# Optimization experiments

Measured on AMD Instinct MI355X. Metric: run time of the kernel, lower is better.

The kernel has to match this reference:

```python
import jax, jax.numpy as jnp
import numpy as np
import math

DIM = 1024
H = 16
HD = DIM // H  # 64
M = 64         # num_features
B, S = 4, 4096


def setup_inputs() -> dict:
    key = jax.random.key(0)
    ks = jax.random.split(key, 10)
    sc = 1.0 / math.sqrt(DIM)
    return {
        "x": jax.random.normal(ks[0], (B, S, DIM), dtype=jnp.float32),
        "Wq": jax.random.normal(ks[1], (DIM, DIM), dtype=jnp.float32) * sc,
        "bq": jax.random.normal(ks[2], (DIM,), dtype=jnp.float32) * 0.01,
        "Wk": jax.random.normal(ks[3], (DIM, DIM), dtype=jnp.float32) * sc,
        "bk": jax.random.normal(ks[4], (DIM,), dtype=jnp.float32) * 0.01,
        "Wv": jax.random.normal(ks[5], (DIM, DIM), dtype=jnp.float32) * sc,
        "bv": jax.random.normal(ks[6], (DIM,), dtype=jnp.float32) * 0.01,
        "Wo": jax.random.normal(ks[7], (DIM, DIM), dtype=jnp.float32) * sc,
        "bo": jax.random.normal(ks[8], (DIM,), dtype=jnp.float32) * 0.01,
        "P": jax.random.normal(ks[9], (H, M, HD), dtype=jnp.float32),
    }


def _feature_map(t, P):
    # t: [b,h,s,d], P: [h,m,d] -> relu(t @ P^T) / sqrt(m)
    proj = jnp.einsum("bhsd,hmd->bhsm", t, P)
    return jax.nn.relu(proj) * (1.0 / math.sqrt(P.shape[1]))


def reference(x, Wq, bq, Wk, bk, Wv, bv, Wo, bo, P):
    b, s, dim = x.shape
    h, m, hd = P.shape
    # Linear projections (torch Linear: x @ W^T + b), split heads -> [b,h,s,hd]
    def split_heads(y):
        return y.reshape(b, s, h, hd).transpose(0, 2, 1, 3)
    q = split_heads(x @ Wq.T + bq)
    k = split_heads(x @ Wk.T + bk)
    v = split_heads(x @ Wv.T + bv)
    q_prime = _feature_map(q, P)  # [b,h,s,m]
    k_prime = _feature_map(k, P)  # [b,h,s,m]
    kv = jnp.einsum("bhsm,bhsd->bhmd", k_prime, v)       # [b,h,m,hd]
    attn = jnp.einsum("bhsm,bhmd->bhsd", q_prime, kv)    # [b,h,s,hd]
    attn = attn.transpose(0, 2, 1, 3).reshape(b, s, dim)
    return attn @ Wo.T + bo
```

## Files before the change

kernel.cpp:

```cpp
#include <hip/hip_runtime.h>
#include <hip/hip_bf16.h>
#include <cstdint>

typedef __bf16 bf16_t;
typedef bf16_t bf16x8 __attribute__((ext_vector_type(8)));
typedef float f32x4 __attribute__((ext_vector_type(4)));

#define BM 128
#define BN 128
#define BKK 32


__device__ __forceinline__ void gload_lds16(const bf16_t* g, bf16_t* l) {
  __builtin_amdgcn_global_load_lds(
      (const __attribute__((address_space(1))) uint32_t*)g,
      (__attribute__((address_space(3))) uint32_t*)l, 16, 0, 0);
}

__global__ void cast_f32_bf16(const float* __restrict__ in, bf16_t* __restrict__ out, int n8) {
  int i = blockIdx.x * 256 + threadIdx.x;
  if (i < n8) {
    const f32x4* p = (const f32x4*)(in + (long)i * 8);
    f32x4 a = p[0], b = p[1];
    bf16x8 o;
#pragma unroll
    for (int j = 0; j < 4; ++j) { o[j] = (bf16_t)a[j]; o[j + 4] = (bf16_t)b[j]; }
    *(bf16x8*)(out + (long)i * 8) = o;
  }
}

__global__ void copy_f32(const float* __restrict__ in, float* __restrict__ out, int n) {
  int i = blockIdx.x * 256 + threadIdx.x;
  if (i < n) out[i] = in[i];
}

__global__ __launch_bounds__(256) void prep_wqk(
    const float* __restrict__ Wq, const float* __restrict__ bq,
    const float* __restrict__ Wk, const float* __restrict__ bk,
    const float* __restrict__ P,
    bf16_t* __restrict__ Wcat, float* __restrict__ bcat)
{
  int bid = blockIdx.x;
  int qk = bid >> 7, h = (bid >> 3) & 15, kt = bid & 7;
  const float* W = qk ? Wk : Wq;
  const float* bias = qk ? bk : bq;
  __shared__ float Pl[64 * 64];
  __shared__ float Wlt[128 * 68];
  int t = threadIdx.x;
  int k0 = kt * 128;
  for (int i = t * 4; i < 4096; i += 1024)
    *(f32x4*)&Pl[i] = *(const f32x4*)&P[h * 4096 + i];
  for (int fi = t; fi < 2048; fi += 256) {
    int row = fi >> 5;
    int c4 = fi & 31;
    f32x4 w = *(const f32x4*)&W[(long)(h * 64 + row) * 1024 + k0 + c4 * 4];
#pragma unroll
    for (int j = 0; j < 4; ++j) Wlt[(c4 * 4 + j) * 68 + row] = w[j];
  }
  __syncthreads();
  int kloc = t >> 1;
  int mh = (t & 1) * 32;
  for (int m = mh; m < mh + 32; ++m) {
    f32x4 s = {0.f, 0.f, 0.f, 0.f};
#pragma unroll
    for (int dd = 0; dd < 16; ++dd)
      s += (*(const f32x4*)&Pl[m * 64 + dd * 4]) * (*(const f32x4*)&Wlt[kloc * 68 + dd * 4]);
    float a = s[0] + s[1] + s[2] + s[3];
    Wcat[(long)(qk * 1024 + h * 64 + m) * 1024 + k0 + kloc] = (bf16_t)a;
  }
  if (kt == 0 && t < 64) {
    float a = 0.f;
    for (int d = 0; d < 64; ++d) a += Pl[t * 64 + d] * bias[h * 64 + d];
    bcat[qk * 1024 + h * 64 + t] = a;
  }
}

template <int EPI>
__global__ __launch_bounds__(256) void gemm_bt(
    const bf16_t* __restrict__ A, int lda,
    const bf16_t* __restrict__ B0, int ldb,
    const float* __restrict__ bias,
    void* __restrict__ Cv, int ldc,
    int K, int rows_per_batch, long bstride)
{
  __shared__ alignas(16) bf16_t As[BM * BKK];
  __shared__ alignas(16) bf16_t Bs[BN * BKK];
  const int tid = threadIdx.x;
  const int wave = tid >> 6, lane = tid & 63;
  const int lhi = lane >> 4, llo = lane & 15;
  const int wr = wave >> 1, wc = wave & 1;
  const int row0 = blockIdx.x * BM, col0 = blockIdx.y * BN;
  const bf16_t* Bm = B0 + (long)(row0 / rows_per_batch) * bstride;

  const int fa = tid * 8;
  const int ra = fa >> 5, ca = fa & 31;
  const long gA0 = (long)(row0 + ra) * lda + ca;
  const long gA1 = (long)(row0 + 64 + ra) * lda + ca;
  const long gB0 = (long)(col0 + ra) * ldb + ca;
  const long gB1 = (long)(col0 + 64 + ra) * ldb + ca;

  f32x4 acc[4][4] = {};

  for (int k0 = 0; k0 < K; k0 += BKK) {
    gload_lds16(A + gA0 + k0, &As[fa]);
    gload_lds16(A + gA1 + k0, &As[fa + 2048]);
    gload_lds16(Bm + gB0 + k0, &Bs[fa]);
    gload_lds16(Bm + gB1 + k0, &Bs[fa + 2048]);
    __syncthreads();
    bf16x8 afr[4], bfr[4];
#pragma unroll
    for (int i = 0; i < 4; ++i) {
      afr[i] = *(const bf16x8*)&As[(wr * 64 + i * 16 + llo) * BKK + lhi * 8];
      bfr[i] = *(const bf16x8*)&Bs[(wc * 64 + i * 16 + llo) * BKK + lhi * 8];
    }
#pragma unroll
    for (int mi = 0; mi < 4; ++mi)
#pragma unroll
      for (int ni = 0; ni < 4; ++ni)
        acc[mi][ni] = __builtin_amdgcn_mfma_f32_16x16x32_bf16(afr[mi], bfr[ni], acc[mi][ni], 0, 0, 0);
    __syncthreads();
  }

#pragma unroll
  for (int ni = 0; ni < 4; ++ni) {
    const int gcol = col0 + wc * 64 + ni * 16 + llo;
    const float bz = bias[gcol];
#pragma unroll
    for (int mi = 0; mi < 4; ++mi) {
      const int grow0 = row0 + wr * 64 + mi * 16 + lhi * 4;
#pragma unroll
      for (int j = 0; j < 4; ++j) {
        float v = acc[mi][ni][j] + bz;
        if constexpr (EPI == 1) { if (gcol < 2048) v = fmaxf(v, 0.f) * 0.125f; }
        if constexpr (EPI == 2)
          ((float*)Cv)[(long)(grow0 + j) * ldc + gcol] = v;
        else
          ((bf16_t*)Cv)[(long)(grow0 + j) * ldc + gcol] = (bf16_t)v;
      }
    }
  }
}

__global__ __launch_bounds__(256) void kv_partial(
    const bf16_t* __restrict__ QKV, float* __restrict__ kvpart)
{
  int bh = blockIdx.x;
  int split = blockIdx.y;
  int b = bh >> 4, h = bh & 15;
  __shared__ alignas(16) bf16_t Kt[64 * 32];
  __shared__ alignas(16) bf16_t Vt[64 * 32];
  int t = threadIdx.x;
  int wv = t >> 6, lane = t & 63, lhi = lane >> 4, llo = lane & 15;
  int r = t >> 3;
  int c = (t & 7) * 8;
  f32x4 acc[4] = {};
  long rowbase = ((long)b * 4096 + split * 512) * 3072 + h * 64 + c;
  for (int sc = 0; sc < 16; ++sc) {
    long off = rowbase + (long)(sc * 32 + r) * 3072;
    bf16x8 kk = *(const bf16x8*)(QKV + off + 1024);
    bf16x8 vvv = *(const bf16x8*)(QKV + off + 2048);
#pragma unroll
    for (int j = 0; j < 8; ++j) {
      Kt[(c + j) * 32 + r] = kk[j];
      Vt[(c + j) * 32 + r] = vvv[j];
    }
    __syncthreads();
    bf16x8 a = *(const bf16x8*)&Kt[(wv * 16 + llo) * 32 + lhi * 8];
#pragma unroll
    for (int ni = 0; ni < 4; ++ni) {
      bf16x8 bb = *(const bf16x8*)&Vt[(ni * 16 + llo) * 32 + lhi * 8];
      acc[ni] = __builtin_amdgcn_mfma_f32_16x16x32_bf16(a, bb, acc[ni], 0, 0, 0);
    }
    __syncthreads();
  }
#pragma unroll
  for (int ni = 0; ni < 4; ++ni)
#pragma unroll
    for (int j = 0; j < 4; ++j) {
      int m = wv * 16 + lhi * 4 + j;
      int d = ni * 16 + llo;
      kvpart[((long)split * 64 + bh) * 4096 + m * 64 + d] = acc[ni][j];
    }
}

__global__ void kv_reduce(const float* __restrict__ part, float* __restrict__ kv) {
  int i = blockIdx.x * 256 + threadIdx.x;
  float s = 0.f;
#pragma unroll
  for (int sp = 0; sp < 8; ++sp) s += part[sp * 262144 + i];
  kv[i] = s;
}

__global__ __launch_bounds__(256) void wcombt_kernel(
    const float* __restrict__ kv, const float* __restrict__ Wo,
    bf16_t* __restrict__ WcT)
{
  int nt = blockIdx.x, h = blockIdx.y, b = blockIdx.z;
  __shared__ float kvs[4096];
  int t = threadIdx.x;
  for (int i = t * 4; i < 4096; i += 1024)
    *(f32x4*)&kvs[i] = *(const f32x4*)&kv[((long)b * 16 + h) * 4096 + i];
  __syncthreads();
  int n = nt * 128 + (t >> 1);
  int mh = (t & 1) * 32;
  f32x4 wo[16];
#pragma unroll
  for (int dd = 0; dd < 16; ++dd) wo[dd] = *(const f32x4*)&Wo[(long)n * 1024 + h * 64 + dd * 4];
  for (int m = mh; m < mh + 32; ++m) {
    f32x4 s = {0.f, 0.f, 0.f, 0.f};
#pragma unroll
    for (int dd = 0; dd < 16; ++dd)
      s += (*(const f32x4*)&kvs[m * 64 + dd * 4]) * wo[dd];
    WcT[((long)b * 1024 + n) * 1024 + h * 64 + m] = (bf16_t)(s[0] + s[1] + s[2] + s[3]);
  }
}

extern "C" void kernel_launch(void* const* d_in, const int* in_sizes, int n_in,
                              void* d_out, int out_size, void* d_ws, size_t ws_size,
                              hipStream_t stream) {
  (void)in_sizes; (void)n_in; (void)out_size; (void)ws_size;
  const float* x  = (const float*)d_in[0];
  const float* Wq = (const float*)d_in[1];
  const float* bq = (const float*)d_in[2];
  const float* Wk = (const float*)d_in[3];
  const float* bk = (const float*)d_in[4];
  const float* Wv = (const float*)d_in[5];
  const float* bv = (const float*)d_in[6];
  const float* Wo = (const float*)d_in[7];
  const float* bo = (const float*)d_in[8];
  const float* P  = (const float*)d_in[9];
  float* out = (float*)d_out;

  char* ws = (char*)d_ws;
  bf16_t* xb     = (bf16_t*)(ws + 0);
  bf16_t* QKV    = (bf16_t*)(ws + 33554432);
  bf16_t* Wcat   = (bf16_t*)(ws + 134217728);
  float*  bcat   = (float*) (ws + 140509184);
  float*  kvpart = (float*) (ws + 140521472);
  float*  kvbuf  = (float*) (ws + 148910080);
  bf16_t* WcT    = (bf16_t*)(ws + 149958656);

  cast_f32_bf16<<<8192, 256, 0, stream>>>(x, xb, 2097152);
  cast_f32_bf16<<<512, 256, 0, stream>>>(Wv, Wcat + (size_t)2048 * 1024, 131072);
  copy_f32<<<4, 256, 0, stream>>>(bv, bcat + 2048, 1024);
  prep_wqk<<<256, 256, 0, stream>>>(Wq, bq, Wk, bk, P, Wcat, bcat);

  gemm_bt<1><<<dim3(128, 24), 256, 0, stream>>>(
      xb, 1024, Wcat, 1024, bcat, QKV, 3072, 1024, 1 << 30, 0);

  kv_partial<<<dim3(64, 8), 256, 0, stream>>>(QKV, kvpart);
  kv_reduce<<<1024, 256, 0, stream>>>(kvpart, kvbuf);

  wcombt_kernel<<<dim3(8, 16, 4), 256, 0, stream>>>(kvbuf, Wo, WcT);

  gemm_bt<2><<<dim3(128, 8), 256, 0, stream>>>(
      QKV, 3072, WcT, 1024, bo, out, 1024, 1024, 4096, (long)1024 * 1024);
}
```

Measured before the change: 287.1 us.

## Replace GEMM with 256x256 double-buffered tiled kernel with swizzled LDS

Replaces the 128x128, single-buffered BK=32 GEMM with a 256x256 tile, 512-thread kernel using BK=64. The kernel double-buffers LDS with async global-to-LDS loads issued during MFMA compute, XOR-swizzles the LDS layout to avoid bank conflicts, and raises wave priority around MFMA bursts. It also remaps block IDs so consecutive blocks are spread across XCDs. The larger tiles give more data reuse and fewer barriers per FLOP, at the cost of higher register and LDS use (128 KB LDS) and fewer blocks, which may hurt occupancy or tail balance on the smaller output GEMM.

```diff
diff --git a/kernel.cpp b/kernel.cpp
--- a/kernel.cpp
+++ b/kernel.cpp
@@ -5,10 +5,6 @@
 typedef __bf16 bf16_t;
 typedef bf16_t bf16x8 __attribute__((ext_vector_type(8)));
 typedef float f32x4 __attribute__((ext_vector_type(4)));
-
-#define BM 128
-#define BN 128
-#define BKK 32
 
 
 __device__ __forceinline__ void gload_lds16(const bf16_t* g, bf16_t* l) {
@@ -76,58 +72,108 @@
 }
 
 template <int EPI>
-__global__ __launch_bounds__(256) void gemm_bt(
+__global__ __launch_bounds__(512, 2) void gemm256(
     const bf16_t* __restrict__ A, int lda,
     const bf16_t* __restrict__ B0, int ldb,
     const float* __restrict__ bias,
     void* __restrict__ Cv, int ldc,
-    int K, int rows_per_batch, long bstride)
+    int K, int ncols, int cpx,
+    int rows_per_batch, long bstride)
 {
-  __shared__ alignas(16) bf16_t As[BM * BKK];
-  __shared__ alignas(16) bf16_t Bs[BN * BKK];
+  __shared__ bf16_t sA[2][16384];
+  __shared__ bf16_t sB[2][16384];
+
+  const int lin = blockIdx.x;
+  const int wgid = (lin & 7) * cpx + (lin >> 3);
+  const int row0 = (wgid / ncols) * 256;
+  const int col0 = (wgid % ncols) * 256;
+
   const int tid = threadIdx.x;
-  const int wave = tid >> 6, lane = tid & 63;
-  const int lhi = lane >> 4, llo = lane & 15;
-  const int wr = wave >> 1, wc = wave & 1;
-  const int row0 = blockIdx.x * BM, col0 = blockIdx.y * BN;
+  const int w = tid >> 6, l = tid & 63;
+  const int wr = w >> 2, wc = w & 3;
+  const int llo = l & 15, lhi = l >> 4;
+  const int x7 = llo & 7;
+
   const bf16_t* Bm = B0 + (long)(row0 / rows_per_batch) * bstride;
 
-  const int fa = tid * 8;
-  const int ra = fa >> 5, ca = fa & 31;
-  const long gA0 = (long)(row0 + ra) * lda + ca;
-  const long gA1 = (long)(row0 + 64 + ra) * lda + ca;
-  const long gB0 = (long)(col0 + ra) * ldb + ca;
-  const long gB1 = (long)(col0 + 64 + ra) * ldb + ca;
-
-  f32x4 acc[4][4] = {};
-
-  for (int k0 = 0; k0 < K; k0 += BKK) {
-    gload_lds16(A + gA0 + k0, &As[fa]);
-    gload_lds16(A + gA1 + k0, &As[fa + 2048]);
-    gload_lds16(Bm + gB0 + k0, &Bs[fa]);
-    gload_lds16(Bm + gB1 + k0, &Bs[fa + 2048]);
-    __syncthreads();
-    bf16x8 afr[4], bfr[4];
-#pragma unroll
-    for (int i = 0; i < 4; ++i) {
-      afr[i] = *(const bf16x8*)&As[(wr * 64 + i * 16 + llo) * BKK + lhi * 8];
-      bfr[i] = *(const bf16x8*)&Bs[(wc * 64 + i * 16 + llo) * BKK + lhi * 8];
-    }
-#pragma unroll
-    for (int mi = 0; mi < 4; ++mi)
-#pragma unroll
-      for (int ni = 0; ni < 4; ++ni)
-        acc[mi][ni] = __builtin_amdgcn_mfma_f32_16x16x32_bf16(afr[mi], bfr[ni], acc[mi][ni], 0, 0, 0);
-    __syncthreads();
-  }
+  long a_off[4], b_off[4];
+#pragma unroll
+  for (int i = 0; i < 4; ++i) {
+    int c = i * 512 + tid;
+    int r = c >> 3;
+    int kqs = (c & 7) ^ (r & 7);
+    a_off[i] = (long)(row0 + r) * lda + kqs * 8;
+    b_off[i] = (long)(col0 + r) * ldb + kqs * 8;
+  }
+  const int ldst = tid * 8;
+
+  const int aoff0 = ((lhi)     ^ x7) * 8;
+  const int aoff1 = ((lhi + 4) ^ x7) * 8;
+  const int abase = (wr * 128 + llo) * 64;
+  const int bbase = (wc * 64 + llo) * 64;
+
+  f32x4 acc[8][4] = {};
+  const int NT = K >> 6;
+
+#pragma unroll
+  for (int i = 0; i < 4; ++i) {
+    gload_lds16(A + a_off[i], &sA[0][i * 4096 + ldst]);
+    gload_lds16(Bm + b_off[i], &sB[0][i * 4096 + ldst]);
+  }
+  __syncthreads();
+
+#define TILE_BODY(PC, PN, T)                                                            \
+  {                                                                                     \
+    bf16x8 bfr[4][2], afr[4][2];                                                        \
+    _Pragma("unroll") for (int ni = 0; ni < 4; ++ni) {                                  \
+      bfr[ni][0] = *(const bf16x8*)&sB[PC][bbase + ni * 1024 + aoff0];                  \
+      bfr[ni][1] = *(const bf16x8*)&sB[PC][bbase + ni * 1024 + aoff1];                  \
+    }                                                                                   \
+    _Pragma("unroll") for (int mi = 0; mi < 4; ++mi) {                                  \
+      afr[mi][0] = *(const bf16x8*)&sA[PC][abase + mi * 1024 + aoff0];                  \
+      afr[mi][1] = *(const bf16x8*)&sA[PC][abase + mi * 1024 + aoff1];                  \
+    }                                                                                   \
+    if ((T) + 1 < NT) {                                                                 \
+      long ks = (long)((T) + 1) * 64;                                                   \
+      _Pragma("unroll") for (int i = 0; i < 4; ++i) {                                   \
+        gload_lds16(A + a_off[i] + ks, &sA[PN][i * 4096 + ldst]);                       \
+        gload_lds16(Bm + b_off[i] + ks, &sB[PN][i * 4096 + ldst]);                      \
+      }                                                                                 \
+    }                                                                                   \
+    __builtin_amdgcn_s_setprio(1);                                                      \
+    _Pragma("unroll") for (int mi = 0; mi < 4; ++mi)                                    \
+      _Pragma("unroll") for (int ni = 0; ni < 4; ++ni) {                                \
+        acc[mi][ni] = __builtin_amdgcn_mfma_f32_16x16x32_bf16(afr[mi][0], bfr[ni][0], acc[mi][ni], 0, 0, 0); \
+        acc[mi][ni] = __builtin_amdgcn_mfma_f32_16x16x32_bf16(afr[mi][1], bfr[ni][1], acc[mi][ni], 0, 0, 0); \
+      }                                                                                 \
+    __builtin_amdgcn_s_setprio(0);                                                      \
+    _Pragma("unroll") for (int mi = 0; mi < 4; ++mi) {                                  \
+      afr[mi][0] = *(const bf16x8*)&sA[PC][abase + (mi + 4) * 1024 + aoff0];            \
+      afr[mi][1] = *(const bf16x8*)&sA[PC][abase + (mi + 4) * 1024 + aoff1];            \
+    }                                                                                   \
+    __builtin_amdgcn_s_setprio(1);                                                      \
+    _Pragma("unroll") for (int mi = 0; mi < 4; ++mi)                                    \
+      _Pragma("unroll") for (int ni = 0; ni < 4; ++ni) {                                \
+        acc[mi + 4][ni] = __builtin_amdgcn_mfma_f32_16x16x32_bf16(afr[mi][0], bfr[ni][0], acc[mi + 4][ni], 0, 0, 0); \
+        acc[mi + 4][ni] = __builtin_amdgcn_mfma_f32_16x16x32_bf16(afr[mi][1], bfr[ni][1], acc[mi + 4][ni], 0, 0, 0); \
+      }                                                                                 \
+    __builtin_amdgcn_s_setprio(0);                                                      \
+    __syncthreads();                                                                    \
+  }
+
+  for (int t = 0; t < NT; t += 2) {
+    TILE_BODY(0, 1, t);
+    TILE_BODY(1, 0, t + 1);
+  }
+#undef TILE_BODY
 
 #pragma unroll
   for (int ni = 0; ni < 4; ++ni) {
     const int gcol = col0 + wc * 64 + ni * 16 + llo;
     const float bz = bias[gcol];
 #pragma unroll
-    for (int mi = 0; mi < 4; ++mi) {
-      const int grow0 = row0 + wr * 64 + mi * 16 + lhi * 4;
+    for (int mi = 0; mi < 8; ++mi) {
+      const int grow0 = row0 + wr * 128 + mi * 16 + lhi * 4;
 #pragma unroll
       for (int j = 0; j < 4; ++j) {
         float v = acc[mi][ni][j] + bz;
@@ -245,14 +291,14 @@
   copy_f32<<<4, 256, 0, stream>>>(bv, bcat + 2048, 1024);
   prep_wqk<<<256, 256, 0, stream>>>(Wq, bq, Wk, bk, P, Wcat, bcat);
 
-  gemm_bt<1><<<dim3(128, 24), 256, 0, stream>>>(
-      xb, 1024, Wcat, 1024, bcat, QKV, 3072, 1024, 1 << 30, 0);
+  gemm256<1><<<768, 512, 0, stream>>>(
+      xb, 1024, Wcat, 1024, bcat, QKV, 3072, 1024, 12, 96, 1 << 30, 0);
 
   kv_partial<<<dim3(64, 8), 256, 0, stream>>>(QKV, kvpart);
   kv_reduce<<<1024, 256, 0, stream>>>(kvpart, kvbuf);
 
   wcombt_kernel<<<dim3(8, 16, 4), 256, 0, stream>>>(kvbuf, Wo, WcT);
 
-  gemm_bt<2><<<dim3(128, 8), 256, 0, stream>>>(
-      QKV, 3072, WcT, 1024, bo, out, 1024, 1024, 4096, (long)1024 * 1024);
-}
+  gemm256<2><<<256, 512, 0, stream>>>(
+      QKV, 3072, WcT, 1024, bo, out, 1024, 1024, 4, 32, 4096, (long)1024 * 1024);
+}
```

Measured after the change: 236.9 us. 17.5% less time.

## Replace GEMM with 256x256 double-buffered, swizzled-LDS, pipelined MFMA kernel

Applied to the files above, without the earlier changes.

Replaces the simple 128x128 single-buffered GEMM, which has two barriers per 32-wide K step, with a 256x256 tile kernel using 512 threads. It uses a 64-wide K step, double-buffered LDS (128 KB), XOR-swizzled LDS layout and staged global->LDS loads interleaved with MFMA phases, using manual waitcnt, barriers and setprio. It also remaps block IDs so groups of 8 consecutive blocks hit different row tiles for better L2/XCD locality. This aims to hide memory latency and raise MFMA utilisation, at the cost of large LDS, high register pressure and fragile hand-tuned synchronisation.

```diff
diff --git a/kernel.cpp b/kernel.cpp
--- a/kernel.cpp
+++ b/kernel.cpp
@@ -5,10 +5,6 @@
 typedef __bf16 bf16_t;
 typedef bf16_t bf16x8 __attribute__((ext_vector_type(8)));
 typedef float f32x4 __attribute__((ext_vector_type(4)));
-
-#define BM 128
-#define BN 128
-#define BKK 32
 
 
 __device__ __forceinline__ void gload_lds16(const bf16_t* g, bf16_t* l) {
@@ -75,59 +71,118 @@
   }
 }
 
+#define VMW(N) asm volatile("s_waitcnt vmcnt(" #N ")" ::: "memory")
+#define LGK(N) asm volatile("s_waitcnt lgkmcnt(" #N ")" ::: "memory")
+#define SBAR() __builtin_amdgcn_s_barrier()
+
+#define STAGE_A(P, H, KT) {                                                  \
+  const bf16_t* s_ = A + aG + (long)(H) * 128 * lda + (KT);                  \
+  gload_lds16(s_, &smem[(P)*16384 + (H)*8192 + dst8]);                       \
+  gload_lds16(s_ + 64 * lda, &smem[(P)*16384 + (H)*8192 + 4096 + dst8]); }
+
+#define STAGE_B(P, H, KT) {                                                  \
+  const bf16_t* s_ = Bm + bG + (long)(H) * 128 * ldb + (KT);                 \
+  gload_lds16(s_, &smem[32768 + (P)*16384 + (H)*8192 + dst8]);               \
+  gload_lds16(s_ + 64 * ldb, &smem[32768 + (P)*16384 + (H)*8192 + 4096 + dst8]); }
+
+#define RD_A(dst, P, QM)                                                     \
+  _Pragma("unroll") for (int i = 0; i < 4; ++i) {                            \
+    dst[i][0] = *(const bf16x8*)&smem[(P)*16384 + aR + ((QM)*64 + i*16)*64 + e0]; \
+    dst[i][1] = *(const bf16x8*)&smem[(P)*16384 + aR + ((QM)*64 + i*16)*64 + e1]; }
+
+#define RD_B(dst, P, QN)                                                     \
+  _Pragma("unroll") for (int j = 0; j < 2; ++j) {                            \
+    dst[j][0] = *(const bf16x8*)&smem[32768 + (P)*16384 + bR + ((QN)*32 + j*16)*64 + e0]; \
+    dst[j][1] = *(const bf16x8*)&smem[32768 + (P)*16384 + bR + ((QN)*32 + j*16)*64 + e1]; }
+
+#define MFMA16(MB, NB, AF, BF) {                                             \
+  __builtin_amdgcn_s_setprio(1);                                             \
+  _Pragma("unroll") for (int i = 0; i < 4; ++i)                              \
+    _Pragma("unroll") for (int j = 0; j < 2; ++j) {                          \
+      acc[(MB)+i][(NB)+j] = __builtin_amdgcn_mfma_f32_16x16x32_bf16(AF[i][0], BF[j][0], acc[(MB)+i][(NB)+j], 0, 0, 0); \
+      acc[(MB)+i][(NB)+j] = __builtin_amdgcn_mfma_f32_16x16x32_bf16(AF[i][1], BF[j][1], acc[(MB)+i][(NB)+j], 0, 0, 0); \
+    }                                                                        \
+  __builtin_amdgcn_s_setprio(0); }
+
+#define TILE(P, KT1, KT2, SB1, S2, WN) {                                     \
+  RD_A(afr0, P, 0); RD_B(bfr0, P, 0);                                        \
+  if (SB1) STAGE_B((P)^1, 1, KT1);                                           \
+  LGK(8); SBAR(); LGK(0);                                                    \
+  MFMA16(0, 0, afr0, bfr0);                                                  \
+  SBAR();                                                                    \
+  RD_A(afr1, P, 1);                                                          \
+  SBAR(); LGK(0);                                                            \
+  MFMA16(4, 0, afr1, bfr0);                                                  \
+  SBAR();                                                                    \
+  RD_B(bfr1, P, 1);                                                          \
+  if (S2) STAGE_A(P, 0, KT2);                                                \
+  SBAR(); LGK(0);                                                            \
+  MFMA16(4, 2, afr1, bfr1);                                                  \
+  SBAR();                                                                    \
+  if (S2) { STAGE_A(P, 1, KT2); STAGE_B(P, 0, KT2); }                        \
+  SBAR();                                                                    \
+  MFMA16(0, 2, afr0, bfr1);                                                  \
+  VMW(WN); SBAR();                                                           \
+}
+
 template <int EPI>
-__global__ __launch_bounds__(256) void gemm_bt(
+__global__ __launch_bounds__(512, 2) void gemm256(
     const bf16_t* __restrict__ A, int lda,
     const bf16_t* __restrict__ B0, int ldb,
     const float* __restrict__ bias,
     void* __restrict__ Cv, int ldc,
-    int K, int rows_per_batch, long bstride)
+    int K, int ncols, int cpx,
+    int rows_per_batch, long bstride)
 {
-  __shared__ alignas(16) bf16_t As[BM * BKK];
-  __shared__ alignas(16) bf16_t Bs[BN * BKK];
+  __shared__ alignas(16) bf16_t smem[65536];
+
+  const int lin = blockIdx.x;
+  const int wgid = (lin & 7) * cpx + (lin >> 3);
+  const int row0 = (wgid / ncols) * 256;
+  const int col0 = (wgid % ncols) * 256;
+
   const int tid = threadIdx.x;
-  const int wave = tid >> 6, lane = tid & 63;
-  const int lhi = lane >> 4, llo = lane & 15;
-  const int wr = wave >> 1, wc = wave & 1;
-  const int row0 = blockIdx.x * BM, col0 = blockIdx.y * BN;
+  const int w = tid >> 6, l = tid & 63;
+  const int wr = w >> 2, wc = w & 3;
+  const int llo = l & 15, lhi = l >> 4;
+  const int x7 = llo & 7;
+
   const bf16_t* Bm = B0 + (long)(row0 / rows_per_batch) * bstride;
 
-  const int fa = tid * 8;
-  const int ra = fa >> 5, ca = fa & 31;
-  const long gA0 = (long)(row0 + ra) * lda + ca;
-  const long gA1 = (long)(row0 + 64 + ra) * lda + ca;
-  const long gB0 = (long)(col0 + ra) * ldb + ca;
-  const long gB1 = (long)(col0 + 64 + ra) * ldb + ca;
-
-  f32x4 acc[4][4] = {};
-
-  for (int k0 = 0; k0 < K; k0 += BKK) {
-    gload_lds16(A + gA0 + k0, &As[fa]);
-    gload_lds16(A + gA1 + k0, &As[fa + 2048]);
-    gload_lds16(Bm + gB0 + k0, &Bs[fa]);
-    gload_lds16(Bm + gB1 + k0, &Bs[fa + 2048]);
-    __syncthreads();
-    bf16x8 afr[4], bfr[4];
-#pragma unroll
-    for (int i = 0; i < 4; ++i) {
-      afr[i] = *(const bf16x8*)&As[(wr * 64 + i * 16 + llo) * BKK + lhi * 8];
-      bfr[i] = *(const bf16x8*)&Bs[(wc * 64 + i * 16 + llo) * BKK + lhi * 8];
-    }
-#pragma unroll
-    for (int mi = 0; mi < 4; ++mi)
-#pragma unroll
-      for (int ni = 0; ni < 4; ++ni)
-        acc[mi][ni] = __builtin_amdgcn_mfma_f32_16x16x32_bf16(afr[mi], bfr[ni], acc[mi][ni], 0, 0, 0);
-    __syncthreads();
-  }
+  const int r0 = tid >> 3;
+  const int kq0 = (tid & 7) ^ (r0 & 7);
+  const long aG = (long)(row0 + r0) * lda + kq0 * 8;
+  const long bG = (long)(col0 + r0) * ldb + kq0 * 8;
+  const int dst8 = tid * 8;
+
+  const int aR = wr * 8192 + llo * 64;
+  const int bR = (wc >> 1) * 8192 + (wc & 1) * 4096 + llo * 64;
+  const int e0 = ((lhi) ^ x7) * 8;
+  const int e1 = ((4 + lhi) ^ x7) * 8;
+
+  f32x4 acc[8][4] = {};
+  bf16x8 afr0[4][2], afr1[4][2], bfr0[2][2], bfr1[2][2];
+  const int NT = K >> 6;
+
+  STAGE_A(0, 0, 0L); STAGE_A(0, 1, 0L); STAGE_B(0, 0, 0L); STAGE_B(0, 1, 0L);
+  STAGE_A(1, 0, 64L); STAGE_A(1, 1, 64L); STAGE_B(1, 0, 64L);
+  VMW(6); SBAR();
+
+  int t = 0;
+  for (; t + 4 <= NT; t += 2) {
+    TILE(0, (long)(t + 1) * 64, (long)(t + 2) * 64, 1, 1, 6);
+    TILE(1, (long)(t + 2) * 64, (long)(t + 3) * 64, 1, 1, 6);
+  }
+  TILE(0, (long)(NT - 1) * 64, 0L, 1, 0, 0);
+  TILE(1, 0L, 0L, 0, 0, 0);
 
 #pragma unroll
   for (int ni = 0; ni < 4; ++ni) {
-    const int gcol = col0 + wc * 64 + ni * 16 + llo;
+    const int gcol = col0 + wc * 64 + (ni >> 1) * 32 + (ni & 1) * 16 + llo;
     const float bz = bias[gcol];
 #pragma unroll
-    for (int mi = 0; mi < 4; ++mi) {
-      const int grow0 = row0 + wr * 64 + mi * 16 + lhi * 4;
+    for (int mi = 0; mi < 8; ++mi) {
+      const int grow0 = row0 + wr * 128 + (mi >> 2) * 64 + (mi & 3) * 16 + lhi * 4;
 #pragma unroll
       for (int j = 0; j < 4; ++j) {
         float v = acc[mi][ni][j] + bz;
@@ -245,14 +300,14 @@
   copy_f32<<<4, 256, 0, stream>>>(bv, bcat + 2048, 1024);
   prep_wqk<<<256, 256, 0, stream>>>(Wq, bq, Wk, bk, P, Wcat, bcat);
 
-  gemm_bt<1><<<dim3(128, 24), 256, 0, stream>>>(
-      xb, 1024, Wcat, 1024, bcat, QKV, 3072, 1024, 1 << 30, 0);
+  gemm256<1><<<768, 512, 0, stream>>>(
+      xb, 1024, Wcat, 1024, bcat, QKV, 3072, 1024, 12, 96, 1 << 30, 0);
 
   kv_partial<<<dim3(64, 8), 256, 0, stream>>>(QKV, kvpart);
   kv_reduce<<<1024, 256, 0, stream>>>(kvpart, kvbuf);
 
   wcombt_kernel<<<dim3(8, 16, 4), 256, 0, stream>>>(kvbuf, Wo, WcT);
 
-  gemm_bt<2><<<dim3(128, 8), 256, 0, stream>>>(
-      QKV, 3072, WcT, 1024, bo, out, 1024, 1024, 4096, (long)1024 * 1024);
-}
+  gemm256<2><<<256, 512, 0, stream>>>(
+      QKV, 3072, WcT, 1024, bo, out, 1024, 1024, 4, 32, 4096, (long)1024 * 1024);
+}
```

New measurement: 309.1 us. 7.7% more time.
